# Kernel tuning notes

Hardware: AMD Instinct MI355X
Metric: run time of the kernel (lower is better)

The kernel has to match this reference:

```python
import jax, jax.numpy as jnp
import numpy as np

N_HEADS = 18
HEAD_DIM = 16
ROPE_THETA = 10000.0
SLIDING_WINDOW = 4096


def _rotate_half(x):
    half = x.shape[-1] // 2
    return jnp.concatenate([-x[..., half:], x[..., :half]], axis=-1)


def setup_inputs() -> dict:
    key = jax.random.key(0)
    k0, k1, k2, k3, k4 = jax.random.split(key, 5)
    B, S, H = 2, 2048, 288
    std = 0.02
    return {
        "hidden_states": jax.random.normal(k0, (B, S, H), dtype=jnp.float32),
        "Wq": jax.random.normal(k1, (H, H), dtype=jnp.float32) * std,
        "Wk": jax.random.normal(k2, (H, H), dtype=jnp.float32) * std,
        "Wv": jax.random.normal(k3, (H, H), dtype=jnp.float32) * std,
        "Wo": jax.random.normal(k4, (H, H), dtype=jnp.float32) * std,
    }


def reference(hidden_states, Wq, Wk, Wv, Wo):
    B, S, H = hidden_states.shape
    nH, D = N_HEADS, HEAD_DIM

    # QKV projections (nn.Linear: y = x @ W.T), reshape to [B, nH, S, D]
    def proj(W):
        return jnp.einsum("bsh,oh->bso", hidden_states, W).reshape(B, S, nH, D).transpose(0, 2, 1, 3)

    q, k, v = proj(Wq), proj(Wk), proj(Wv)

    # Rotary embedding: position_ids = arange(S)
    pos = jnp.arange(S, dtype=jnp.float32)
    inv_freq = 1.0 / (ROPE_THETA ** (jnp.arange(0, D, 2, dtype=jnp.float32) / D))
    freqs = pos[:, None] * inv_freq[None, :]            # [S, D/2]
    emb = jnp.concatenate([freqs, freqs], axis=-1)      # [S, D]
    cos = jnp.cos(emb)[None, None, :, :]                # [1, 1, S, D]
    sin = jnp.sin(emb)[None, None, :, :]
    q = q * cos + _rotate_half(q) * sin
    k = k * cos + _rotate_half(k) * sin

    # num_key_value_groups = 1 -> repeat_kv is identity.
    scores = jnp.einsum("bhqd,bhkd->bhqk", q, k) / jnp.sqrt(jnp.float32(D))

    # Sliding-window causal mask: attend iff 0 <= i - j < window
    i = jnp.arange(S)[:, None]
    j = jnp.arange(S)[None, :]
    allowed = (j <= i) & (i - j < SLIDING_WINDOW)       # [S, S]
    neg = jnp.finfo(scores.dtype).min
    scores = jnp.where(allowed[None, None, :, :], scores, neg)

    attn = jax.nn.softmax(scores.astype(jnp.float32), axis=-1).astype(q.dtype)
    out = jnp.einsum("bhqk,bhkd->bhqd", attn, v)        # [B, nH, S, D]
    out = out.transpose(0, 2, 1, 3).reshape(B, S, H)
    return jnp.einsum("bsh,oh->bso", out, Wo)
```

## Files before the change

### kernel.cpp

```cpp
#include <hip/hip_runtime.h>
#include <hip/hip_bf16.h>
#include <math.h>

#define H_DIM 288
#define NHEADS 18
#define HEAD_D 16
#define SEQ 2048
#define BATCH 2
#define M_TOT (BATCH*SEQ)
#define XCNT (M_TOT*H_DIM)
#define WCNT (H_DIM*H_DIM)
#define NUNITS 10368
#define NQUNITS 2304

typedef _Float16 f16_t;
typedef __attribute__((ext_vector_type(2))) _Float16 half2v;
typedef __attribute__((ext_vector_type(4))) _Float16 half4v;
typedef __attribute__((ext_vector_type(8))) _Float16 half8v;
typedef __attribute__((ext_vector_type(4))) float   float4v;

__global__ __launch_bounds__(256) void cvt_f16(
    const float* __restrict__ X,
    const float* __restrict__ Wq, const float* __restrict__ Wk,
    const float* __restrict__ Wv, const float* __restrict__ Wo,
    f16_t* __restrict__ Xf, f16_t* __restrict__ Wf)
{
    int idx = blockIdx.x * 256 + threadIdx.x;
    const int X4 = XCNT/4, W4 = WCNT/4;
    if (idx >= X4 + 4*W4) return;
    const float* src; f16_t* dst; int off;
    if (idx < X4) { src = X; dst = Xf; off = idx; }
    else {
        int r = idx - X4;
        int wz = r / W4; off = r - wz*W4;
        src = (wz==0) ? Wq : (wz==1) ? Wk : (wz==2) ? Wv : Wo;
        dst = Wf + (size_t)wz*WCNT;
    }
    float4 v = ((const float4*)src)[off];
    half4v h; h[0]=(f16_t)v.x; h[1]=(f16_t)v.y; h[2]=(f16_t)v.z; h[3]=(f16_t)v.w;
    ((half4v*)dst)[off] = h;
}

__global__ __launch_bounds__(64) void qkv_mfma(
    const f16_t* __restrict__ Xf, const f16_t* __restrict__ Wf,
    f16_t* __restrict__ Q16, f16_t* __restrict__ K16, f16_t* __restrict__ Vt)
{
    const int bx = blockIdx.x;
    const int z  = bx/6;
    const int n0 = (bx - z*6)*48;
    const int m0 = blockIdx.y*32;
    const int lane = threadIdx.x & 63;
    const int n = lane & 15, quad = lane >> 4;

    const f16_t* W = Wf + (size_t)z*WCNT;

    float4v acc[2][3];
    #pragma unroll
    for (int mt = 0; mt < 2; mt++)
        #pragma unroll
        for (int nt = 0; nt < 3; nt++)
            acc[mt][nt] = (float4v){0.f,0.f,0.f,0.f};

    for (int k0 = 0; k0 < H_DIM; k0 += 32) {
        half8v a[2], b[3];
        #pragma unroll
        for (int mt = 0; mt < 2; mt++)
            a[mt] = *(const half8v*)(Xf + (size_t)(m0 + mt*16 + n)*H_DIM + k0 + quad*8);
        #pragma unroll
        for (int nt = 0; nt < 3; nt++)
            b[nt] = *(const half8v*)(W + (size_t)(n0 + nt*16 + n)*H_DIM + k0 + quad*8);
        #pragma unroll
        for (int mt = 0; mt < 2; mt++)
            #pragma unroll
            for (int nt = 0; nt < 3; nt++)
                acc[mt][nt] = __builtin_amdgcn_mfma_f32_16x16x32_f16(a[mt], b[nt], acc[mt][nt], 0, 0, 0);
    }

    if (z < 2) {
        f16_t* dst = (z == 0) ? Q16 : K16;
        const float invf_rev = exp2f(-1.6609640474436813f * (float)(n & 7))
                             * 0.15915494309189535f;
        #pragma unroll
        for (int mt = 0; mt < 2; mt++) {
            #pragma unroll
            for (int r = 0; r < 4; r++) {
                int m = m0 + mt*16 + quad*4 + r;
                int bb = m >> 11, s = m & (SEQ - 1);
                float rev = (float)s * invf_rev;
                float fr = rev - floorf(rev);
                float sn = __builtin_amdgcn_sinf(fr);
                float c  = __builtin_amdgcn_cosf(fr);
                #pragma unroll
                for (int nt = 0; nt < 3; nt++) {
                    float own = acc[mt][nt][r];
                    float par = __shfl_xor(own, 8, 64);
                    float val = (n & 8) ? fmaf(own, c, par*sn) : fmaf(own, c, -par*sn);
                    if (z == 0) val *= 0.36067376022224085f;
                    int head = (n0 >> 4) + nt;
                    dst[((size_t)((bb*NHEADS + head)*SEQ) + s)*HEAD_D + n] = (f16_t)val;
                }
            }
        }
    } else {
        #pragma unroll
        for (int mt = 0; mt < 2; mt++)
            #pragma unroll
            for (int nt = 0; nt < 3; nt++)
                #pragma unroll
                for (int r = 0; r < 4; r++) {
                    int m = m0 + mt*16 + quad*4 + r;
                    int bb = m >> 11, s = m & (SEQ - 1);
                    int head = (n0 >> 4) + nt;
                    Vt[(size_t)(bb*NHEADS + head)*(SEQ*HEAD_D)
                       + (size_t)(s >> 4)*256 + n*16 + (s & 15)] = (f16_t)acc[mt][nt][r];
                }
    }
}

__device__ __forceinline__ half4v pack4(const float p[4]) {
    half2v ab = __builtin_bit_cast(half2v, __builtin_amdgcn_cvt_pkrtz(p[0], p[1]));
    half2v cd = __builtin_bit_cast(half2v, __builtin_amdgcn_cvt_pkrtz(p[2], p[3]));
    half4v o; o[0]=ab[0]; o[1]=ab[1]; o[2]=cd[0]; o[3]=cd[1];
    return o;
}

__global__ __launch_bounds__(256) void attn_part(
    const f16_t* __restrict__ Q16, const f16_t* __restrict__ K16,
    const f16_t* __restrict__ Vt,
    float4* __restrict__ accbuf, float* __restrict__ lbuf)
{
    const int unit = blockIdx.x*4 + (threadIdx.x >> 6);
    const int lane = threadIdx.x & 63;
    const int n = lane & 15, quad = lane >> 4;

    const int bh = unit / 288;
    const int rem = unit - bh*288;
    int g, t0;
    if      (rem < 8)   { g=0; t0=rem;     }
    else if (rem < 24)  { g=1; t0=rem-8;   }
    else if (rem < 48)  { g=2; t0=rem-24;  }
    else if (rem < 80)  { g=3; t0=rem-48;  }
    else if (rem < 120) { g=4; t0=rem-80;  }
    else if (rem < 168) { g=5; t0=rem-120; }
    else if (rem < 224) { g=6; t0=rem-168; }
    else                { g=7; t0=rem-224; }
    const int qd = t0 / (g+1);
    const int qp = 8*g + qd;
    const int chunk = t0 - qd*(g+1);
    const int q0 = qp*32;

    half4v qb0 = *(const half4v*)(Q16 + ((size_t)bh*SEQ + q0 + n)*HEAD_D + quad*4);
    half4v qb1 = *(const half4v*)(Q16 + ((size_t)bh*SEQ + q0 + 16 + n)*HEAD_D + quad*4);
    const f16_t* Kb = K16 + (size_t)bh * SEQ * HEAD_D;
    const f16_t* Vb = Vt  + (size_t)bh * SEQ * HEAD_D;
    const int loff = n*16 + quad*4;

    const float4v zero = {0.f, 0.f, 0.f, 0.f};
    float4v acc0 = zero, acc1 = zero;
    float l0 = 0.f, l1 = 0.f;

    const int lim0 = 2*qp, lim1 = 2*qp + 1;
    const int ktlo = chunk*16;
    const int kthi = min(ktlo + 15, lim1);

    if (ktlo + 15 < lim0) {
        half4v KA[16], VA[16];
        #pragma unroll
        for (int i = 0; i < 16; i++) {
            KA[i] = *(const half4v*)(Kb + (size_t)(ktlo + i)*256 + loff);
            VA[i] = *(const half4v*)(Vb + (size_t)(ktlo + i)*256 + loff);
        }
        #pragma unroll
        for (int i = 0; i < 16; i++) {
            float4v s1 = __builtin_amdgcn_mfma_f32_16x16x16f16(KA[i], qb1, zero, 0, 0, 0);
            float4v s0 = __builtin_amdgcn_mfma_f32_16x16x16f16(KA[i], qb0, zero, 0, 0, 0);
            float p1[4], p0[4];
            #pragma unroll
            for (int r = 0; r < 4; r++) { p1[r] = __builtin_amdgcn_exp2f(s1[r]); p0[r] = __builtin_amdgcn_exp2f(s0[r]); }
            l1 += (p1[0]+p1[1]) + (p1[2]+p1[3]);
            l0 += (p0[0]+p0[1]) + (p0[2]+p0[3]);
            acc1 = __builtin_amdgcn_mfma_f32_16x16x16f16(VA[i], pack4(p1), acc1, 0, 0, 0);
            acc0 = __builtin_amdgcn_mfma_f32_16x16x16f16(VA[i], pack4(p0), acc0, 0, 0, 0);
        }
    } else {
        int kt = ktlo;
        half4v ka = *(const half4v*)(Kb + (size_t)kt*256 + loff);
        half4v va = *(const half4v*)(Vb + (size_t)kt*256 + loff);
        for (; kt <= kthi; kt++) {
            half4v kan, van;
            if (kt < kthi) {
                kan = *(const half4v*)(Kb + (size_t)(kt+1)*256 + loff);
                van = *(const half4v*)(Vb + (size_t)(kt+1)*256 + loff);
            }
            {
                float4v s = __builtin_amdgcn_mfma_f32_16x16x16f16(ka, qb1, zero, 0, 0, 0);
                float p[4];
                #pragma unroll
                for (int r = 0; r < 4; r++) {
                    float e = __builtin_amdgcn_exp2f(s[r]);
                    p[r] = (kt == lim1 && quad*4 + r > n) ? 0.0f : e;
                }
                l1 += (p[0]+p[1]) + (p[2]+p[3]);
                acc1 = __builtin_amdgcn_mfma_f32_16x16x16f16(va, pack4(p), acc1, 0, 0, 0);
            }
            if (kt <= lim0) {
                float4v s = __builtin_amdgcn_mfma_f32_16x16x16f16(ka, qb0, zero, 0, 0, 0);
                float p[4];
                #pragma unroll
                for (int r = 0; r < 4; r++) {
                    float e = __builtin_amdgcn_exp2f(s[r]);
                    p[r] = (kt == lim0 && quad*4 + r > n) ? 0.0f : e;
                }
                l0 += (p[0]+p[1]) + (p[2]+p[3]);
                acc0 = __builtin_amdgcn_mfma_f32_16x16x16f16(va, pack4(p), acc0, 0, 0, 0);
            }
            ka = kan; va = van;
        }
    }

    float4 a0; a0.x=acc0[0]; a0.y=acc0[1]; a0.z=acc0[2]; a0.w=acc0[3];
    float4 a1; a1.x=acc1[0]; a1.y=acc1[1]; a1.z=acc1[2]; a1.w=acc1[3];
    accbuf[((size_t)unit*2 + 0)*64 + lane] = a0;
    accbuf[((size_t)unit*2 + 1)*64 + lane] = a1;
    lbuf[((size_t)unit*2 + 0)*64 + lane] = l0;
    lbuf[((size_t)unit*2 + 1)*64 + lane] = l1;
}

__global__ __launch_bounds__(256) void attn_red(
    const float4* __restrict__ accbuf, const float* __restrict__ lbuf,
    f16_t* __restrict__ Of)
{
    const int wid = blockIdx.x*4 + (threadIdx.x >> 6);
    const int lane = threadIdx.x & 63;
    const int n = lane & 15, quad = lane >> 4;
    const int bh = wid >> 6, qp = wid & 63;
    const int b = bh / NHEADS, h = bh - b*NHEADS;
    const int g = qp >> 3, j = qp & 7;
    const int nch = g + 1;
    const int ubase = bh*288 + qp + 4*g*(g-1) + g*j;

    #pragma unroll
    for (int t = 0; t < 2; t++) {
        float4 a = {0.f, 0.f, 0.f, 0.f};
        float l = 0.f;
        for (int c = 0; c < nch; c++) {
            size_t idx = ((size_t)(ubase + c)*2 + t)*64 + lane;
            float4 v = accbuf[idx];
            a.x += v.x; a.y += v.y; a.z += v.z; a.w += v.w;
            l += lbuf[idx];
        }
        l += __shfl_xor(l, 16, 64);
        l += __shfl_xor(l, 32, 64);
        float inv = 1.0f / l;
        half4v o;
        o[0]=(f16_t)(a.x*inv); o[1]=(f16_t)(a.y*inv);
        o[2]=(f16_t)(a.z*inv); o[3]=(f16_t)(a.w*inv);
        *(half4v*)(Of + (size_t)(b*SEQ + qp*32 + t*16 + n)*H_DIM + h*HEAD_D + quad*4) = o;
    }
}

__global__ __launch_bounds__(64) void out_mfma(
    const f16_t* __restrict__ Of, const f16_t* __restrict__ Wo16,
    float* __restrict__ C)
{
    const int n0 = blockIdx.x * 48;
    const int m0 = blockIdx.y * 32;
    const int lane = threadIdx.x & 63;
    const int n = lane & 15, quad = lane >> 4;

    float4v acc[2][3];
    #pragma unroll
    for (int mt = 0; mt < 2; mt++)
        #pragma unroll
        for (int nt = 0; nt < 3; nt++)
            acc[mt][nt] = (float4v){0.f,0.f,0.f,0.f};

    for (int k0 = 0; k0 < H_DIM; k0 += 32) {
        half8v a[2], b[3];
        #pragma unroll
        for (int mt = 0; mt < 2; mt++)
            a[mt] = *(const half8v*)(Of + (size_t)(m0 + mt*16 + n)*H_DIM + k0 + quad*8);
        #pragma unroll
        for (int nt = 0; nt < 3; nt++)
            b[nt] = *(const half8v*)(Wo16 + (size_t)(n0 + nt*16 + n)*H_DIM + k0 + quad*8);
        #pragma unroll
        for (int mt = 0; mt < 2; mt++)
            #pragma unroll
            for (int nt = 0; nt < 3; nt++)
                acc[mt][nt] = __builtin_amdgcn_mfma_f32_16x16x32_f16(a[mt], b[nt], acc[mt][nt], 0, 0, 0);
    }
    #pragma unroll
    for (int mt = 0; mt < 2; mt++)
        #pragma unroll
        for (int nt = 0; nt < 3; nt++)
            #pragma unroll
            for (int r = 0; r < 4; r++) {
                int m = m0 + mt*16 + quad*4 + r;
                C[(size_t)m*H_DIM + n0 + nt*16 + n] = acc[mt][nt][r];
            }
}

extern "C" void kernel_launch(void* const* d_in, const int* in_sizes, int n_in,
                              void* d_out, int out_size, void* d_ws, size_t ws_size,
                              hipStream_t stream)
{
    const float* Xh = (const float*)d_in[0];
    const float* Wq = (const float*)d_in[1];
    const float* Wk = (const float*)d_in[2];
    const float* Wv = (const float*)d_in[3];
    const float* Wo = (const float*)d_in[4];
    float* out = (float*)d_out;

    f16_t* Xf  = (f16_t*)d_ws;
    f16_t* Wf  = Xf + XCNT;
    f16_t* Q16 = Wf + 4*(size_t)WCNT;
    f16_t* K16 = Q16 + XCNT;
    f16_t* Vt  = K16 + XCNT;
    f16_t* Of  = Vt + XCNT;
    float4* accbuf = (float4*)(Of + XCNT);
    float*  lbuf   = (float*)(accbuf + (size_t)NUNITS*2*64);

    const int total4 = (XCNT + 4*WCNT)/4;
    cvt_f16<<<dim3((total4 + 255)/256), 256, 0, stream>>>(Xh, Wq, Wk, Wv, Wo, Xf, Wf);
    qkv_mfma<<<dim3(18, 128), 64, 0, stream>>>(Xf, Wf, Q16, K16, Vt);
    attn_part<<<dim3(NUNITS/4), 256, 0, stream>>>(Q16, K16, Vt, accbuf, lbuf);
    attn_red<<<dim3(NQUNITS/4), 256, 0, stream>>>(accbuf, lbuf, Of);
    out_mfma<<<dim3(6, 128), 64, 0, stream>>>(Of, Wf + 3*(size_t)WCNT, out);
}
```

Baseline: 112.4 us.

## Fuse split-KV attention partials and reduction into one per-query-tile kernel

Replaces the split-K attention (partial kernel writing per-chunk accumulators and row sums to a workspace, then a separate reduction kernel) with a single kernel where each 64-thread block loops over all key chunks for its 32-query tile and normalizes in registers. Blocks are ordered longest-first, with the query tile reversed and blocks interleaved across heads, to balance the causal triangle. It also raises wave priority around the dense MFMA section. This removes the partial-buffer global traffic and one launch, but loses key-dimension parallelism, so the largest tiles become serial chains of up to eight chunks.

```diff
diff --git a/kernel.cpp b/kernel.cpp
--- a/kernel.cpp
+++ b/kernel.cpp
@@ -10,7 +10,6 @@
 #define M_TOT (BATCH*SEQ)
 #define XCNT (M_TOT*H_DIM)
 #define WCNT (H_DIM*H_DIM)
-#define NUNITS 10368
 #define NQUNITS 2304
 
 typedef _Float16 f16_t;
@@ -124,30 +123,18 @@
     return o;
 }
 
-__global__ __launch_bounds__(256) void attn_part(
+__global__ __launch_bounds__(64) void attn_fused(
     const f16_t* __restrict__ Q16, const f16_t* __restrict__ K16,
-    const f16_t* __restrict__ Vt,
-    float4* __restrict__ accbuf, float* __restrict__ lbuf)
-{
-    const int unit = blockIdx.x*4 + (threadIdx.x >> 6);
+    const f16_t* __restrict__ Vt, f16_t* __restrict__ Of)
+{
+    const int bid = blockIdx.x;
+    const int u   = (bid & 7) * 288 + (bid >> 3);
+    const int bh  = u >> 6;
+    const int qp  = 63 - (u & 63);
     const int lane = threadIdx.x & 63;
     const int n = lane & 15, quad = lane >> 4;
-
-    const int bh = unit / 288;
-    const int rem = unit - bh*288;
-    int g, t0;
-    if      (rem < 8)   { g=0; t0=rem;     }
-    else if (rem < 24)  { g=1; t0=rem-8;   }
-    else if (rem < 48)  { g=2; t0=rem-24;  }
-    else if (rem < 80)  { g=3; t0=rem-48;  }
-    else if (rem < 120) { g=4; t0=rem-80;  }
-    else if (rem < 168) { g=5; t0=rem-120; }
-    else if (rem < 224) { g=6; t0=rem-168; }
-    else                { g=7; t0=rem-224; }
-    const int qd = t0 / (g+1);
-    const int qp = 8*g + qd;
-    const int chunk = t0 - qd*(g+1);
     const int q0 = qp*32;
+    const int b = bh / NHEADS, h = bh - b*NHEADS;
 
     half4v qb0 = *(const half4v*)(Q16 + ((size_t)bh*SEQ + q0 + n)*HEAD_D + quad*4);
     half4v qb1 = *(const half4v*)(Q16 + ((size_t)bh*SEQ + q0 + 16 + n)*HEAD_D + quad*4);
@@ -160,103 +147,78 @@
     float l0 = 0.f, l1 = 0.f;
 
     const int lim0 = 2*qp, lim1 = 2*qp + 1;
-    const int ktlo = chunk*16;
-    const int kthi = min(ktlo + 15, lim1);
-
-    if (ktlo + 15 < lim0) {
-        half4v KA[16], VA[16];
-        #pragma unroll
-        for (int i = 0; i < 16; i++) {
-            KA[i] = *(const half4v*)(Kb + (size_t)(ktlo + i)*256 + loff);
-            VA[i] = *(const half4v*)(Vb + (size_t)(ktlo + i)*256 + loff);
+    const int nchunk = (qp >> 3) + 1;
+
+    for (int chunk = 0; chunk < nchunk; chunk++) {
+        const int ktlo = chunk*16;
+        if (ktlo + 15 < lim0) {
+            half4v KA[16], VA[16];
+            #pragma unroll
+            for (int i = 0; i < 16; i++) {
+                KA[i] = *(const half4v*)(Kb + (size_t)(ktlo + i)*256 + loff);
+                VA[i] = *(const half4v*)(Vb + (size_t)(ktlo + i)*256 + loff);
+            }
+            __builtin_amdgcn_s_setprio(1);
+            #pragma unroll
+            for (int i = 0; i < 16; i++) {
+                float4v s1 = __builtin_amdgcn_mfma_f32_16x16x16f16(KA[i], qb1, zero, 0, 0, 0);
+                float4v s0 = __builtin_amdgcn_mfma_f32_16x16x16f16(KA[i], qb0, zero, 0, 0, 0);
+                float p1[4], p0[4];
+                #pragma unroll
+                for (int r = 0; r < 4; r++) { p1[r] = __builtin_amdgcn_exp2f(s1[r]); p0[r] = __builtin_amdgcn_exp2f(s0[r]); }
+                l1 += (p1[0]+p1[1]) + (p1[2]+p1[3]);
+                l0 += (p0[0]+p0[1]) + (p0[2]+p0[3]);
+                acc1 = __builtin_amdgcn_mfma_f32_16x16x16f16(VA[i], pack4(p1), acc1, 0, 0, 0);
+                acc0 = __builtin_amdgcn_mfma_f32_16x16x16f16(VA[i], pack4(p0), acc0, 0, 0, 0);
+            }
+            __builtin_amdgcn_s_setprio(0);
+        } else {
+            const int kthi = min(ktlo + 15, lim1);
+            int kt = ktlo;
+            half4v ka = *(const half4v*)(Kb + (size_t)kt*256 + loff);
+            half4v va = *(const half4v*)(Vb + (size_t)kt*256 + loff);
+            for (; kt <= kthi; kt++) {
+                half4v kan, van;
+                if (kt < kthi) {
+                    kan = *(const half4v*)(Kb + (size_t)(kt+1)*256 + loff);
+                    van = *(const half4v*)(Vb + (size_t)(kt+1)*256 + loff);
+                }
+                {
+                    float4v s = __builtin_amdgcn_mfma_f32_16x16x16f16(ka, qb1, zero, 0, 0, 0);
+                    float p[4];
+                    #pragma unroll
+                    for (int r = 0; r < 4; r++) {
+                        float e = __builtin_amdgcn_exp2f(s[r]);
+                        p[r] = (kt == lim1 && quad*4 + r > n) ? 0.0f : e;
+                    }
+                    l1 += (p[0]+p[1]) + (p[2]+p[3]);
+                    acc1 = __builtin_amdgcn_mfma_f32_16x16x16f16(va, pack4(p), acc1, 0, 0, 0);
+                }
+                if (kt <= lim0) {
+                    float4v s = __builtin_amdgcn_mfma_f32_16x16x16f16(ka, qb0, zero, 0, 0, 0);
+                    float p[4];
+                    #pragma unroll
+                    for (int r = 0; r < 4; r++) {
+                        float e = __builtin_amdgcn_exp2f(s[r]);
+                        p[r] = (kt == lim0 && quad*4 + r > n) ? 0.0f : e;
+                    }
+                    l0 += (p[0]+p[1]) + (p[2]+p[3]);
+                    acc0 = __builtin_amdgcn_mfma_f32_16x16x16f16(va, pack4(p), acc0, 0, 0, 0);
+                }
+                ka = kan; va = van;
+            }
         }
-        #pragma unroll
-        for (int i = 0; i < 16; i++) {
-            float4v s1 = __builtin_amdgcn_mfma_f32_16x16x16f16(KA[i], qb1, zero, 0, 0, 0);
-            float4v s0 = __builtin_amdgcn_mfma_f32_16x16x16f16(KA[i], qb0, zero, 0, 0, 0);
-            float p1[4], p0[4];
-            #pragma unroll
-            for (int r = 0; r < 4; r++) { p1[r] = __builtin_amdgcn_exp2f(s1[r]); p0[r] = __builtin_amdgcn_exp2f(s0[r]); }
-            l1 += (p1[0]+p1[1]) + (p1[2]+p1[3]);
-            l0 += (p0[0]+p0[1]) + (p0[2]+p0[3]);
-            acc1 = __builtin_amdgcn_mfma_f32_16x16x16f16(VA[i], pack4(p1), acc1, 0, 0, 0);
-            acc0 = __builtin_amdgcn_mfma_f32_16x16x16f16(VA[i], pack4(p0), acc0, 0, 0, 0);
-        }
-    } else {
-        int kt = ktlo;
-        half4v ka = *(const half4v*)(Kb + (size_t)kt*256 + loff);
-        half4v va = *(const half4v*)(Vb + (size_t)kt*256 + loff);
-        for (; kt <= kthi; kt++) {
-            half4v kan, van;
-            if (kt < kthi) {
-                kan = *(const half4v*)(Kb + (size_t)(kt+1)*256 + loff);
-                van = *(const half4v*)(Vb + (size_t)(kt+1)*256 + loff);
-            }
-            {
-                float4v s = __builtin_amdgcn_mfma_f32_16x16x16f16(ka, qb1, zero, 0, 0, 0);
-                float p[4];
-                #pragma unroll
-                for (int r = 0; r < 4; r++) {
-                    float e = __builtin_amdgcn_exp2f(s[r]);
-                    p[r] = (kt == lim1 && quad*4 + r > n) ? 0.0f : e;
-                }
-                l1 += (p[0]+p[1]) + (p[2]+p[3]);
-                acc1 = __builtin_amdgcn_mfma_f32_16x16x16f16(va, pack4(p), acc1, 0, 0, 0);
-            }
-            if (kt <= lim0) {
-                float4v s = __builtin_amdgcn_mfma_f32_16x16x16f16(ka, qb0, zero, 0, 0, 0);
-                float p[4];
-                #pragma unroll
-                for (int r = 0; r < 4; r++) {
-                    float e = __builtin_amdgcn_exp2f(s[r]);
-                    p[r] = (kt == lim0 && quad*4 + r > n) ? 0.0f : e;
-                }
-                l0 += (p[0]+p[1]) + (p[2]+p[3]);
-                acc0 = __builtin_amdgcn_mfma_f32_16x16x16f16(va, pack4(p), acc0, 0, 0, 0);
-            }
-            ka = kan; va = van;
-        }
-    }
-
-    float4 a0; a0.x=acc0[0]; a0.y=acc0[1]; a0.z=acc0[2]; a0.w=acc0[3];
-    float4 a1; a1.x=acc1[0]; a1.y=acc1[1]; a1.z=acc1[2]; a1.w=acc1[3];
-    accbuf[((size_t)unit*2 + 0)*64 + lane] = a0;
-    accbuf[((size_t)unit*2 + 1)*64 + lane] = a1;
-    lbuf[((size_t)unit*2 + 0)*64 + lane] = l0;
-    lbuf[((size_t)unit*2 + 1)*64 + lane] = l1;
-}
-
-__global__ __launch_bounds__(256) void attn_red(
-    const float4* __restrict__ accbuf, const float* __restrict__ lbuf,
-    f16_t* __restrict__ Of)
-{
-    const int wid = blockIdx.x*4 + (threadIdx.x >> 6);
-    const int lane = threadIdx.x & 63;
-    const int n = lane & 15, quad = lane >> 4;
-    const int bh = wid >> 6, qp = wid & 63;
-    const int b = bh / NHEADS, h = bh - b*NHEADS;
-    const int g = qp >> 3, j = qp & 7;
-    const int nch = g + 1;
-    const int ubase = bh*288 + qp + 4*g*(g-1) + g*j;
-
-    #pragma unroll
-    for (int t = 0; t < 2; t++) {
-        float4 a = {0.f, 0.f, 0.f, 0.f};
-        float l = 0.f;
-        for (int c = 0; c < nch; c++) {
-            size_t idx = ((size_t)(ubase + c)*2 + t)*64 + lane;
-            float4 v = accbuf[idx];
-            a.x += v.x; a.y += v.y; a.z += v.z; a.w += v.w;
-            l += lbuf[idx];
-        }
-        l += __shfl_xor(l, 16, 64);
-        l += __shfl_xor(l, 32, 64);
-        float inv = 1.0f / l;
-        half4v o;
-        o[0]=(f16_t)(a.x*inv); o[1]=(f16_t)(a.y*inv);
-        o[2]=(f16_t)(a.z*inv); o[3]=(f16_t)(a.w*inv);
-        *(half4v*)(Of + (size_t)(b*SEQ + qp*32 + t*16 + n)*H_DIM + h*HEAD_D + quad*4) = o;
-    }
+    }
+
+    l0 += __shfl_xor(l0, 16, 64); l0 += __shfl_xor(l0, 32, 64);
+    l1 += __shfl_xor(l1, 16, 64); l1 += __shfl_xor(l1, 32, 64);
+    const float inv0 = 1.0f / l0, inv1 = 1.0f / l1;
+
+    half4v o0, o1;
+    #pragma unroll
+    for (int r = 0; r < 4; r++) { o0[r] = (f16_t)(acc0[r]*inv0); o1[r] = (f16_t)(acc1[r]*inv1); }
+    *(half4v*)(Of + (size_t)(b*SEQ + q0 +      n)*H_DIM + h*HEAD_D + quad*4) = o0;
+    *(half4v*)(Of + (size_t)(b*SEQ + q0 + 16 + n)*H_DIM + h*HEAD_D + quad*4) = o1;
 }
 
 __global__ __launch_bounds__(64) void out_mfma(
@@ -317,13 +279,10 @@
     f16_t* K16 = Q16 + XCNT;
     f16_t* Vt  = K16 + XCNT;
     f16_t* Of  = Vt + XCNT;
-    float4* accbuf = (float4*)(Of + XCNT);
-    float*  lbuf   = (float*)(accbuf + (size_t)NUNITS*2*64);
 
     const int total4 = (XCNT + 4*WCNT)/4;
     cvt_f16<<<dim3((total4 + 255)/256), 256, 0, stream>>>(Xh, Wq, Wk, Wv, Wo, Xf, Wf);
     qkv_mfma<<<dim3(18, 128), 64, 0, stream>>>(Xf, Wf, Q16, K16, Vt);
-    attn_part<<<dim3(NUNITS/4), 256, 0, stream>>>(Q16, K16, Vt, accbuf, lbuf);
-    attn_red<<<dim3(NQUNITS/4), 256, 0, stream>>>(accbuf, lbuf, Of);
+    attn_fused<<<dim3(NQUNITS), 64, 0, stream>>>(Q16, K16, Vt, Of);
     out_mfma<<<dim3(6, 128), 64, 0, stream>>>(Of, Wf + 3*(size_t)WCNT, out);
 }
```

New measurement: 118.2 us. 5.1% more time.
